# Performance work log

Measured on AMD Instinct MI355X. Metric: run time of the kernel, lower is better.

## Reference

```python
import jax, jax.numpy as jnp
import numpy as np

LN_EPS = 1e-5


def setup_inputs() -> dict:
    key = jax.random.key(0)
    k1, k2, k3, k4, k5 = jax.random.split(key, 5)
    V, D_REAL, D_HID, D_MODEL = 32000, 768, 512, 4096
    B, S = 4, 2048
    return {
        "real": jax.random.normal(k1, (V, D_REAL), dtype=jnp.float32),
        "llama_embed": jax.random.normal(k2, (V, D_MODEL), dtype=jnp.float32),
        "w1": jax.random.normal(k3, (D_HID, D_REAL), dtype=jnp.float32),  # trans_1.weight
        "w2": jax.random.normal(k4, (D_MODEL, D_HID), dtype=jnp.float32),  # trans_2.weight
        "ln_w": jnp.ones((D_HID,), dtype=jnp.float32),
        "ln_b": jnp.zeros((D_HID,), dtype=jnp.float32),
        "input_ids": jax.random.randint(k5, (B, S), 0, V, dtype=jnp.int64),
    }


def _layernorm(x, w, b):
    mu = jnp.mean(x, axis=-1, keepdims=True)
    var = jnp.mean(jnp.square(x - mu), axis=-1, keepdims=True)
    return (x - mu) * jax.lax.rsqrt(var + LN_EPS) * w + b


def reference(real, llama_embed, w1, w2, ln_w, ln_b, input_ids):
    # trans_2(ELU(LayerNorm(trans_1(real)))) over the FULL table, as in the original
    h = jnp.einsum("vd,hd->vh", real, w1)            # [V, 512]
    h = jax.nn.elu(_layernorm(h, ln_w, ln_b))        # [V, 512]
    transfered = jnp.einsum("vh,mh->vm", h, w2)      # [V, 4096]
    # gather rows per token and add frozen llama embeddings
    return transfered[input_ids] + llama_embed[input_ids]  # [B, S, 4096]
```

## Files before the change

kernel.cpp:

```cpp
#include <hip/hip_runtime.h>
#include <hip/hip_bf16.h>
#include <math.h>

#define TOKENS 8192
#define D_REAL 768
#define D_HID  512
#define D_MODEL 4096

typedef __attribute__((ext_vector_type(8))) short bf16x8;
typedef __attribute__((ext_vector_type(4))) float f32x4;

__device__ inline unsigned short f2bf(float f) {
    union { float f; unsigned u; } v; v.f = f;
    unsigned r = v.u + 0x7FFFu + ((v.u >> 16) & 1u);
    return (unsigned short)(r >> 16);
}
__device__ inline float bf2f(unsigned short h) {
    union { unsigned u; float f; } v; v.u = ((unsigned)h) << 16;
    return v.f;
}

__device__ inline void gload_lds16(const void* g, void* lds_wave_base) {
    __builtin_amdgcn_global_load_lds(
        (const __attribute__((address_space(1))) unsigned*)g,
        (__attribute__((address_space(3))) unsigned*)lds_wave_base,
        16, 0, 0);
}

__global__ __launch_bounds__(256)
void gemm1_mfma(const unsigned short* __restrict__ A,
                const unsigned short* __restrict__ B,
                unsigned short* __restrict__ C)
{
    constexpr int K = D_REAL, N = D_HID;
    __shared__ __align__(16) unsigned short As[64 * 32];
    __shared__ __align__(16) unsigned short Bs[128 * 32];

    const int tid = threadIdx.x;
    const int rowBase = blockIdx.x * 64;
    const int colBase = blockIdx.y * 128;

    const int srow = tid >> 2;
    const int scol = (tid & 3) * 8;
    const unsigned short* gA = A + (size_t)(rowBase + srow) * K + scol;
    const unsigned short* gB = B + (size_t)(colBase + srow) * K + scol;
    unsigned short* lA = As + (tid >> 6) * 512;
    unsigned short* lB = Bs + (tid >> 6) * 512;

    const int lane = tid & 63;
    const int wv   = tid >> 6;
    const int wm   = (wv >> 1) * 32;
    const int wn   = (wv & 1) * 64;
    const int frow = lane & 15;
    const int fk   = (lane >> 4) * 8;

    f32x4 acc[2][4];
    #pragma unroll
    for (int i = 0; i < 2; i++)
        #pragma unroll
        for (int j = 0; j < 4; j++) acc[i][j] = (f32x4)0.f;

    for (int k0 = 0; k0 < K; k0 += 32) {
        gload_lds16(gA,                lA);
        gload_lds16(gB,                lB);
        gload_lds16(gB + (size_t)64*K, lB + 2048);
        gA += 32; gB += 32;
        __syncthreads();

        bf16x8 af[2], bg[4];
        #pragma unroll
        for (int i = 0; i < 2; i++)
            af[i] = *reinterpret_cast<const bf16x8*>(&As[(wm + i*16 + frow) * 32 + fk]);
        #pragma unroll
        for (int j = 0; j < 4; j++)
            bg[j] = *reinterpret_cast<const bf16x8*>(&Bs[(wn + j*16 + frow) * 32 + fk]);

        #pragma unroll
        for (int i = 0; i < 2; i++)
            #pragma unroll
            for (int j = 0; j < 4; j++)
                acc[i][j] = __builtin_amdgcn_mfma_f32_16x16x32_bf16(af[i], bg[j], acc[i][j], 0, 0, 0);
        __syncthreads();
    }

    const int orow0 = wm + (lane >> 4) * 4;
    const int ocol0 = wn + frow;
    #pragma unroll
    for (int i = 0; i < 2; i++)
        #pragma unroll
        for (int r = 0; r < 4; r++) {
            unsigned short* dst = C + (size_t)(rowBase + orow0 + i*16 + r) * N + colBase + ocol0;
            #pragma unroll
            for (int j = 0; j < 4; j++)
                dst[j * 16] = f2bf(acc[i][j][r]);
        }
}

__global__ __launch_bounds__(256)
void gemm2_mfma(const unsigned short* __restrict__ A,
                const unsigned short* __restrict__ B,
                const int* __restrict__ ids,
                const float* __restrict__ embed,
                float* __restrict__ C)
{
    constexpr int K = D_HID, N = D_MODEL;
    __shared__ __align__(16) unsigned short As[128 * 32];
    __shared__ __align__(16) unsigned short Bs[128 * 32];
    __shared__ int sIds[128];

    const int f   = blockIdx.x;
    const int xcd = f & 7;
    const int idx = f >> 3;
    const int rowBase = (xcd * 8 + (idx & 7)) * 128;
    const int colBase = (idx >> 3) * 128;

    const int tid = threadIdx.x;
    if (tid < 128) sIds[tid] = ids[rowBase + tid];

    const int srow = tid >> 2;
    const int scol = (tid & 3) * 8;
    const unsigned short* gA = A + (size_t)(rowBase + srow) * K + scol;
    const unsigned short* gB = B + (size_t)(colBase + srow) * K + scol;
    unsigned short* lA = As + (tid >> 6) * 512;
    unsigned short* lB = Bs + (tid >> 6) * 512;

    const int lane = tid & 63;
    const int wv   = tid >> 6;
    const int wm   = (wv >> 1) * 64;
    const int wn   = (wv & 1) * 64;
    const int frow = lane & 15;
    const int fk   = (lane >> 4) * 8;

    f32x4 acc[4][4];
    #pragma unroll
    for (int i = 0; i < 4; i++)
        #pragma unroll
        for (int j = 0; j < 4; j++) acc[i][j] = (f32x4)0.f;

    for (int k0 = 0; k0 < K; k0 += 32) {
        gload_lds16(gA,                lA);
        gload_lds16(gA + (size_t)64*K, lA + 2048);
        gload_lds16(gB,                lB);
        gload_lds16(gB + (size_t)64*K, lB + 2048);
        gA += 32; gB += 32;
        __syncthreads();

        bf16x8 af[4], bg[4];
        #pragma unroll
        for (int i = 0; i < 4; i++)
            af[i] = *reinterpret_cast<const bf16x8*>(&As[(wm + i*16 + frow) * 32 + fk]);
        #pragma unroll
        for (int j = 0; j < 4; j++)
            bg[j] = *reinterpret_cast<const bf16x8*>(&Bs[(wn + j*16 + frow) * 32 + fk]);

        #pragma unroll
        for (int i = 0; i < 4; i++)
            #pragma unroll
            for (int j = 0; j < 4; j++)
                acc[i][j] = __builtin_amdgcn_mfma_f32_16x16x32_bf16(af[i], bg[j], acc[i][j], 0, 0, 0);
        __syncthreads();
    }

    const int orow0 = wm + (lane >> 4) * 4;
    const int ocol0 = wn + frow;
    #pragma unroll
    for (int i = 0; i < 4; i++) {
        #pragma unroll
        for (int r = 0; r < 4; r++) {
            const int lrow = orow0 + i * 16 + r;
            const size_t grow = (size_t)(rowBase + lrow);
            const float* e = embed + (size_t)sIds[lrow] * N + colBase + ocol0;
            #pragma unroll
            for (int j = 0; j < 4; j++)
                C[grow * N + colBase + ocol0 + j * 16] = acc[i][j][r] + e[j * 16];
        }
    }
}

__global__ __launch_bounds__(256)
void convert2_bf16(const float* __restrict__ s1, unsigned short* __restrict__ d1, int n1,
                   const float* __restrict__ s2, unsigned short* __restrict__ d2, int n2)
{
    int i = blockIdx.x * 256 + threadIdx.x;
    const float* src; unsigned short* dst;
    if (i < n1) { src = s1; dst = d1; }
    else {
        i -= n1;
        if (i >= n2) return;
        src = s2; dst = d2;
    }
    const float4 v = reinterpret_cast<const float4*>(src)[i];
    ushort4 o;
    o.x = f2bf(v.x); o.y = f2bf(v.y); o.z = f2bf(v.z); o.w = f2bf(v.w);
    reinterpret_cast<ushort4*>(dst)[i] = o;
}

__global__ __launch_bounds__(192)
void gather_bf16(const float* __restrict__ real, const int* __restrict__ ids,
                 unsigned short* __restrict__ Ag)
{
    const int row = blockIdx.x;
    const int t = threadIdx.x;
    const float4 v = *reinterpret_cast<const float4*>(real + (size_t)ids[row] * D_REAL + t * 4);
    ushort4 o;
    o.x = f2bf(v.x); o.y = f2bf(v.y); o.z = f2bf(v.z); o.w = f2bf(v.w);
    *reinterpret_cast<ushort4*>(Ag + (size_t)row * D_REAL + t * 4) = o;
}

__global__ __launch_bounds__(256)
void ln_elu_bf16(unsigned short* __restrict__ H,
                 const float* __restrict__ ln_w, const float* __restrict__ ln_b)
{
    const int row = blockIdx.x * 4 + (threadIdx.x >> 6);
    const int t = threadIdx.x & 63;
    unsigned short* x = H + (size_t)row * D_HID + t * 8;

    bf16x8 v = *reinterpret_cast<const bf16x8*>(x);
    float f[8], s = 0.f, ss = 0.f;
    #pragma unroll
    for (int j = 0; j < 8; j++) {
        f[j] = bf2f((unsigned short)v[j]);
        s += f[j]; ss += f[j] * f[j];
    }
    #pragma unroll
    for (int off = 32; off > 0; off >>= 1) {
        s  += __shfl_down(s, off);
        ss += __shfl_down(ss, off);
    }
    s = __shfl(s, 0); ss = __shfl(ss, 0);
    const float mu = s * (1.f / D_HID);
    const float var = ss * (1.f / D_HID) - mu * mu;
    const float rstd = rsqrtf(var + 1e-5f);

    const float4 w0 = *reinterpret_cast<const float4*>(ln_w + t * 8);
    const float4 w1 = *reinterpret_cast<const float4*>(ln_w + t * 8 + 4);
    const float4 b0 = *reinterpret_cast<const float4*>(ln_b + t * 8);
    const float4 b1 = *reinterpret_cast<const float4*>(ln_b + t * 8 + 4);
    const float wa[8] = { w0.x, w0.y, w0.z, w0.w, w1.x, w1.y, w1.z, w1.w };
    const float ba[8] = { b0.x, b0.y, b0.z, b0.w, b1.x, b1.y, b1.z, b1.w };

    bf16x8 o;
    #pragma unroll
    for (int j = 0; j < 8; j++) {
        float y = (f[j] - mu) * rstd * wa[j] + ba[j];
        y = y > 0.f ? y : expm1f(y);
        o[j] = (short)f2bf(y);
    }
    *reinterpret_cast<bf16x8*>(x) = o;
}

extern "C" void kernel_launch(void* const* d_in, const int* in_sizes, int n_in,
                              void* d_out, int out_size, void* d_ws, size_t ws_size,
                              hipStream_t stream)
{
    const float* real  = (const float*)d_in[0];
    const float* embed = (const float*)d_in[1];
    const float* w1    = (const float*)d_in[2];
    const float* w2    = (const float*)d_in[3];
    const float* ln_w  = (const float*)d_in[4];
    const float* ln_b  = (const float*)d_in[5];
    const int*   ids   = (const int*)d_in[6];
    float* out = (float*)d_out;

    unsigned short* Hb  = (unsigned short*)d_ws;
    unsigned short* w1b = Hb  + (size_t)TOKENS * D_HID;
    unsigned short* w2b = w1b + (size_t)D_HID * D_REAL;
    unsigned short* Ag  = (unsigned short*)d_out;

    const int n1 = D_HID * D_REAL / 4, n2 = D_MODEL * D_HID / 4;
    convert2_bf16<<<(n1 + n2 + 255) / 256, 256, 0, stream>>>(w1, w1b, n1, w2, w2b, n2);
    gather_bf16<<<TOKENS, 192, 0, stream>>>(real, ids, Ag);

    dim3 g1(TOKENS / 64, D_HID / 128);
    gemm1_mfma<<<g1, 256, 0, stream>>>(Ag, w1b, Hb);

    ln_elu_bf16<<<TOKENS / 4, 256, 0, stream>>>(Hb, ln_w, ln_b);

    gemm2_mfma<<<2048, 256, 0, stream>>>(Hb, w2b, ids, embed, out);
}
```

Measured before the change: 129.0 us.

## Rewrite gemm2 as 256x256 tile, double-buffered, swizzled-LDS phased MFMA pipeline

Replaces the 128x128 single-buffered gemm2 with a 512-thread kernel that computes 256x256 output tiles. K-tiles of 64 are double-buffered in LDS with an XOR swizzle, and global-to-LDS loads for the next tile are split into four phases interleaved with MFMA bursts, using manual vmcnt waits and s_setprio. The aim is to hide global load latency, cut LDS bank conflicts and raise data reuse per block. It uses 128KB of LDS per block and many accumulator registers, which limits occupancy, and with only 512 blocks the grid gives a thin tail on the GPU.

```diff
diff --git a/kernel.cpp b/kernel.cpp
--- a/kernel.cpp
+++ b/kernel.cpp
@@ -25,6 +25,12 @@
         (const __attribute__((address_space(1))) unsigned*)g,
         (__attribute__((address_space(3))) unsigned*)lds_wave_base,
         16, 0, 0);
+}
+
+__device__ inline void BAR() {
+    asm volatile("" ::: "memory");
+    __builtin_amdgcn_s_barrier();
+    asm volatile("" ::: "memory");
 }
 
 __global__ __launch_bounds__(256)
@@ -96,83 +102,130 @@
         }
 }
 
-__global__ __launch_bounds__(256)
-void gemm2_mfma(const unsigned short* __restrict__ A,
-                const unsigned short* __restrict__ B,
-                const int* __restrict__ ids,
-                const float* __restrict__ embed,
-                float* __restrict__ C)
-{
-    constexpr int K = D_HID, N = D_MODEL;
-    __shared__ __align__(16) unsigned short As[128 * 32];
-    __shared__ __align__(16) unsigned short Bs[128 * 32];
-    __shared__ int sIds[128];
+__global__ __launch_bounds__(512, 2)
+void gemm2_8phase(const unsigned short* __restrict__ A,
+                  const unsigned short* __restrict__ B,
+                  const int* __restrict__ ids,
+                  const float* __restrict__ embed,
+                  float* __restrict__ C)
+{
+    constexpr int K = D_HID, N = D_MODEL, NKT = K / 64;
+    __shared__ __align__(16) unsigned short lds[65536];
+    __shared__ int sIds[256];
+    unsigned short* Alds = lds;
+    unsigned short* Blds = lds + 32768;
 
     const int f   = blockIdx.x;
     const int xcd = f & 7;
     const int idx = f >> 3;
-    const int rowBase = (xcd * 8 + (idx & 7)) * 128;
-    const int colBase = (idx >> 3) * 128;
-
-    const int tid = threadIdx.x;
-    if (tid < 128) sIds[tid] = ids[rowBase + tid];
-
-    const int srow = tid >> 2;
-    const int scol = (tid & 3) * 8;
-    const unsigned short* gA = A + (size_t)(rowBase + srow) * K + scol;
-    const unsigned short* gB = B + (size_t)(colBase + srow) * K + scol;
-    unsigned short* lA = As + (tid >> 6) * 512;
-    unsigned short* lB = Bs + (tid >> 6) * 512;
-
+    const int rowBase = (xcd * 4 + (idx & 3)) * 256;
+    const int colBase = (idx >> 2) * 256;
+
+    const int tid  = threadIdx.x;
     const int lane = tid & 63;
     const int wv   = tid >> 6;
-    const int wm   = (wv >> 1) * 64;
-    const int wn   = (wv & 1) * 64;
+    const int wr   = wv >> 2;
+    const int wc   = wv & 3;
     const int frow = lane & 15;
-    const int fk   = (lane >> 4) * 8;
-
-    f32x4 acc[4][4];
-    #pragma unroll
-    for (int i = 0; i < 4; i++)
+    const int fq   = lane >> 4;
+
+    if (tid < 256) sIds[tid] = ids[rowBase + tid];
+
+    auto STAGE_HALF = [&](const unsigned short* Mp, unsigned short* Ml,
+                          int tileBase, int kt, int h) {
+        const int buf = kt & 1;
+        #pragma unroll
+        for (int u = 0; u < 2; ++u) {
+            const int c    = u * 512 + tid;
+            const int row  = c >> 3;
+            const int slot = (c & 7) ^ (row & 7);
+            const unsigned short* g = Mp + (size_t)(tileBase + h * 128 + row) * K
+                                         + kt * 64 + slot * 8;
+            unsigned short* l = Ml + (buf * 2 + h) * 8192 + (u * 512 + wv * 64) * 8;
+            gload_lds16(g, l);
+        }
+    };
+    auto STAGE = [&](int kt_s, int h_s) {
+        if (kt_s >= NKT) return;
+        if (h_s < 2) STAGE_HALF(A, Alds, rowBase, kt_s, h_s);
+        else         STAGE_HALF(B, Blds, colBase, kt_s, h_s - 2);
+    };
+    auto LDA = [&](int buf, int mf, int kk) -> bf16x8 {
+        const int row  = mf * 16 + frow;
+        const int slot = (kk * 4 + fq) ^ (row & 7);
+        return *reinterpret_cast<const bf16x8*>(
+            Alds + (buf * 2 + wr) * 8192 + row * 64 + slot * 8);
+    };
+    auto LDB = [&](int buf, int nf, int kk) -> bf16x8 {
+        const int rb   = wc * 64 + nf * 16 + frow;
+        const int row  = rb & 127;
+        const int slot = (kk * 4 + fq) ^ (row & 7);
+        return *reinterpret_cast<const bf16x8*>(
+            Blds + (buf * 2 + (rb >> 7)) * 8192 + row * 64 + slot * 8);
+    };
+
+    f32x4 acc[8][4];
+    #pragma unroll
+    for (int i = 0; i < 8; i++)
         #pragma unroll
         for (int j = 0; j < 4; j++) acc[i][j] = (f32x4)0.f;
 
-    for (int k0 = 0; k0 < K; k0 += 32) {
-        gload_lds16(gA,                lA);
-        gload_lds16(gA + (size_t)64*K, lA + 2048);
-        gload_lds16(gB,                lB);
-        gload_lds16(gB + (size_t)64*K, lB + 2048);
-        gA += 32; gB += 32;
-        __syncthreads();
-
-        bf16x8 af[4], bg[4];
-        #pragma unroll
-        for (int i = 0; i < 4; i++)
-            af[i] = *reinterpret_cast<const bf16x8*>(&As[(wm + i*16 + frow) * 32 + fk]);
-        #pragma unroll
-        for (int j = 0; j < 4; j++)
-            bg[j] = *reinterpret_cast<const bf16x8*>(&Bs[(wn + j*16 + frow) * 32 + fk]);
-
-        #pragma unroll
-        for (int i = 0; i < 4; i++)
-            #pragma unroll
-            for (int j = 0; j < 4; j++)
-                acc[i][j] = __builtin_amdgcn_mfma_f32_16x16x32_bf16(af[i], bg[j], acc[i][j], 0, 0, 0);
-        __syncthreads();
-    }
-
-    const int orow0 = wm + (lane >> 4) * 4;
-    const int ocol0 = wn + frow;
-    #pragma unroll
-    for (int i = 0; i < 4; i++) {
-        #pragma unroll
-        for (int r = 0; r < 4; r++) {
-            const int lrow = orow0 + i * 16 + r;
-            const size_t grow = (size_t)(rowBase + lrow);
-            const float* e = embed + (size_t)sIds[lrow] * N + colBase + ocol0;
-            #pragma unroll
-            for (int j = 0; j < 4; j++)
-                C[grow * N + colBase + ocol0 + j * 16] = acc[i][j][r] + e[j * 16];
+    STAGE(0, 0); STAGE(0, 1); STAGE(0, 2); STAGE(0, 3); STAGE(1, 0);
+    asm volatile("s_waitcnt vmcnt(2)" ::: "memory");
+    __builtin_amdgcn_s_barrier();
+    asm volatile("" ::: "memory");
+
+    #pragma unroll
+    for (int kt = 0; kt < NKT; ++kt) {
+        const int buf = kt & 1;
+        bf16x8 bg[4][2];
+        #pragma unroll
+        for (int p = 0; p < 4; ++p) {
+            bf16x8 af[2][2];
+            #pragma unroll
+            for (int i = 0; i < 2; ++i)
+                #pragma unroll
+                for (int kk = 0; kk < 2; ++kk)
+                    af[i][kk] = LDA(buf, p * 2 + i, kk);
+            if (p == 0) {
+                #pragma unroll
+                for (int nf = 0; nf < 4; ++nf)
+                    #pragma unroll
+                    for (int kk = 0; kk < 2; ++kk)
+                        bg[nf][kk] = LDB(buf, nf, kk);
+            }
+            if (p < 3) STAGE(kt + 1, p + 1);
+            BAR();
+            if (p == 3) STAGE(kt + 2, 0);
+            __builtin_amdgcn_s_setprio(1);
+            #pragma unroll
+            for (int i = 0; i < 2; ++i)
+                #pragma unroll
+                for (int nf = 0; nf < 4; ++nf)
+                    #pragma unroll
+                    for (int kk = 0; kk < 2; ++kk)
+                        acc[p*2+i][nf] = __builtin_amdgcn_mfma_f32_16x16x32_bf16(
+                            af[i][kk], bg[nf][kk], acc[p*2+i][nf], 0, 0, 0);
+            __builtin_amdgcn_s_setprio(0);
+            if (p == 3) {
+                if (kt + 2 < NKT)      asm volatile("s_waitcnt vmcnt(2)" ::: "memory");
+                else if (kt + 1 < NKT) asm volatile("s_waitcnt vmcnt(0)" ::: "memory");
+            }
+            BAR();
+        }
+    }
+
+    const int ocol0 = colBase + wc * 64 + frow;
+    #pragma unroll
+    for (int mf = 0; mf < 8; ++mf) {
+        #pragma unroll
+        for (int r = 0; r < 4; ++r) {
+            const int lrow = wr * 128 + mf * 16 + fq * 4 + r;
+            const float* e = embed + (size_t)sIds[lrow] * N + ocol0;
+            float* o = C + (size_t)(rowBase + lrow) * N + ocol0;
+            #pragma unroll
+            for (int nf = 0; nf < 4; ++nf)
+                o[nf * 16] = acc[mf][nf][r] + e[nf * 16];
         }
     }
 }
@@ -216,11 +269,11 @@
     unsigned short* x = H + (size_t)row * D_HID + t * 8;
 
     bf16x8 v = *reinterpret_cast<const bf16x8*>(x);
-    float f[8], s = 0.f, ss = 0.f;
+    float fv[8], s = 0.f, ss = 0.f;
     #pragma unroll
     for (int j = 0; j < 8; j++) {
-        f[j] = bf2f((unsigned short)v[j]);
-        s += f[j]; ss += f[j] * f[j];
+        fv[j] = bf2f((unsigned short)v[j]);
+        s += fv[j]; ss += fv[j] * fv[j];
     }
     #pragma unroll
     for (int off = 32; off > 0; off >>= 1) {
@@ -242,7 +295,7 @@
     bf16x8 o;
     #pragma unroll
     for (int j = 0; j < 8; j++) {
-        float y = (f[j] - mu) * rstd * wa[j] + ba[j];
+        float y = (fv[j] - mu) * rstd * wa[j] + ba[j];
         y = y > 0.f ? y : expm1f(y);
         o[j] = (short)f2bf(y);
     }
@@ -276,5 +329,5 @@
 
     ln_elu_bf16<<<TOKENS / 4, 256, 0, stream>>>(Hb, ln_w, ln_b);
 
-    gemm2_mfma<<<2048, 256, 0, stream>>>(Hb, w2b, ids, embed, out);
-}
+    gemm2_8phase<<<512, 512, 0, stream>>>(Hb, w2b, ids, embed, out);
+}
```

After: 124.3 us. -3.6%, faster.

## Fuse token gather into GEMM1 and enlarge GEMM2 tile to 256x128

Applied to the files above, without the earlier changes.

The separate gather/convert kernel is removed. GEMM1 now reads the fp32 rows of `real` selected by the ids directly, converts them to bf16 and stores them in LDS, which saves one launch and a full round trip of the intermediate buffer. GEMM2 moves from 128x128 to 256x128 tiles with 8x4 MFMA fragments per wave and launch_bounds(256,2), so the B tiles are reused more. The larger tile raises register pressure and halves the block count, which may hurt occupancy. The fused A load in GEMM1 goes through registers instead of async global-to-LDS, so it is no longer overlapped with the other loads.

```diff
diff --git a/kernel.cpp b/kernel.cpp
--- a/kernel.cpp
+++ b/kernel.cpp
@@ -18,6 +18,14 @@
 __device__ inline float bf2f(unsigned short h) {
     union { unsigned u; float f; } v; v.u = ((unsigned)h) << 16;
     return v.f;
+}
+__device__ inline bf16x8 cvt8(float4 a, float4 b) {
+    bf16x8 r;
+    r[0] = (short)f2bf(a.x); r[1] = (short)f2bf(a.y);
+    r[2] = (short)f2bf(a.z); r[3] = (short)f2bf(a.w);
+    r[4] = (short)f2bf(b.x); r[5] = (short)f2bf(b.y);
+    r[6] = (short)f2bf(b.z); r[7] = (short)f2bf(b.w);
+    return r;
 }
 
 __device__ inline void gload_lds16(const void* g, void* lds_wave_base) {
@@ -28,17 +36,98 @@
 }
 
 __global__ __launch_bounds__(256)
-void gemm1_mfma(const unsigned short* __restrict__ A,
+void gemm1_mfma(const float* __restrict__ real, const int* __restrict__ ids,
                 const unsigned short* __restrict__ B,
                 unsigned short* __restrict__ C)
 {
     constexpr int K = D_REAL, N = D_HID;
     __shared__ __align__(16) unsigned short As[64 * 32];
     __shared__ __align__(16) unsigned short Bs[128 * 32];
+    __shared__ int sIds[64];
 
     const int tid = threadIdx.x;
     const int rowBase = blockIdx.x * 64;
     const int colBase = blockIdx.y * 128;
+
+    if (tid < 64) sIds[tid] = ids[rowBase + tid];
+    __syncthreads();
+
+    const int srow = tid >> 2;
+    const int scol = (tid & 3) * 8;
+    const float* gA = real + (size_t)sIds[srow] * K + scol;
+    const unsigned short* gB = B + (size_t)(colBase + srow) * K + scol;
+    unsigned short* lB = Bs + (tid >> 6) * 512;
+
+    const int lane = tid & 63;
+    const int wv   = tid >> 6;
+    const int wm   = (wv >> 1) * 32;
+    const int wn   = (wv & 1) * 64;
+    const int frow = lane & 15;
+    const int fk   = (lane >> 4) * 8;
+
+    f32x4 acc[2][4];
+    #pragma unroll
+    for (int i = 0; i < 2; i++)
+        #pragma unroll
+        for (int j = 0; j < 4; j++) acc[i][j] = (f32x4)0.f;
+
+    for (int k0 = 0; k0 < K; k0 += 32) {
+        gload_lds16(gB + k0,                lB);
+        gload_lds16(gB + k0 + (size_t)64*K, lB + 2048);
+        const float4 a0 = *reinterpret_cast<const float4*>(gA + k0);
+        const float4 a1 = *reinterpret_cast<const float4*>(gA + k0 + 4);
+        *reinterpret_cast<bf16x8*>(&As[srow * 32 + scol]) = cvt8(a0, a1);
+        __syncthreads();
+
+        bf16x8 af[2], bg[4];
+        #pragma unroll
+        for (int i = 0; i < 2; i++)
+            af[i] = *reinterpret_cast<const bf16x8*>(&As[(wm + i*16 + frow) * 32 + fk]);
+        #pragma unroll
+        for (int j = 0; j < 4; j++)
+            bg[j] = *reinterpret_cast<const bf16x8*>(&Bs[(wn + j*16 + frow) * 32 + fk]);
+
+        #pragma unroll
+        for (int i = 0; i < 2; i++)
+            #pragma unroll
+            for (int j = 0; j < 4; j++)
+                acc[i][j] = __builtin_amdgcn_mfma_f32_16x16x32_bf16(af[i], bg[j], acc[i][j], 0, 0, 0);
+        __syncthreads();
+    }
+
+    const int orow0 = wm + (lane >> 4) * 4;
+    const int ocol0 = wn + frow;
+    #pragma unroll
+    for (int i = 0; i < 2; i++)
+        #pragma unroll
+        for (int r = 0; r < 4; r++) {
+            unsigned short* dst = C + (size_t)(rowBase + orow0 + i*16 + r) * N + colBase + ocol0;
+            #pragma unroll
+            for (int j = 0; j < 4; j++)
+                dst[j * 16] = f2bf(acc[i][j][r]);
+        }
+}
+
+__global__ __launch_bounds__(256, 2)
+void gemm2_mfma(const unsigned short* __restrict__ A,
+                const unsigned short* __restrict__ B,
+                const int* __restrict__ ids,
+                const float* __restrict__ embed,
+                float* __restrict__ C)
+{
+    constexpr int K = D_HID, N = D_MODEL;
+    __shared__ __align__(16) unsigned short As[256 * 32];
+    __shared__ __align__(16) unsigned short Bs[128 * 32];
+    __shared__ int sIds[256];
+
+    const int f   = blockIdx.x;
+    const int xcd = f & 7;
+    const int idx = f >> 3;
+    const int rowBase = (xcd * 4 + (idx & 3)) * 256;
+    const int colBase = (idx >> 2) * 128;
+
+    const int tid = threadIdx.x;
+    sIds[tid] = ids[rowBase + tid];
 
     const int srow = tid >> 2;
     const int scol = (tid & 3) * 8;
@@ -49,130 +138,56 @@
 
     const int lane = tid & 63;
     const int wv   = tid >> 6;
-    const int wm   = (wv >> 1) * 32;
+    const int wm   = (wv >> 1) * 128;
     const int wn   = (wv & 1) * 64;
     const int frow = lane & 15;
-    const int fk   = (lane >> 4) * 8;
-
-    f32x4 acc[2][4];
-    #pragma unroll
-    for (int i = 0; i < 2; i++)
+    const int fq   = lane >> 4;
+    const int fk   = fq * 8;
+
+    f32x4 acc[8][4];
+    #pragma unroll
+    for (int i = 0; i < 8; i++)
         #pragma unroll
         for (int j = 0; j < 4; j++) acc[i][j] = (f32x4)0.f;
 
     for (int k0 = 0; k0 < K; k0 += 32) {
-        gload_lds16(gA,                lA);
-        gload_lds16(gB,                lB);
-        gload_lds16(gB + (size_t)64*K, lB + 2048);
+        gload_lds16(gA,                 lA);
+        gload_lds16(gA + (size_t)64*K,  lA + 2048);
+        gload_lds16(gA + (size_t)128*K, lA + 4096);
+        gload_lds16(gA + (size_t)192*K, lA + 6144);
+        gload_lds16(gB,                 lB);
+        gload_lds16(gB + (size_t)64*K,  lB + 2048);
         gA += 32; gB += 32;
         __syncthreads();
 
-        bf16x8 af[2], bg[4];
-        #pragma unroll
-        for (int i = 0; i < 2; i++)
-            af[i] = *reinterpret_cast<const bf16x8*>(&As[(wm + i*16 + frow) * 32 + fk]);
-        #pragma unroll
-        for (int j = 0; j < 4; j++)
-            bg[j] = *reinterpret_cast<const bf16x8*>(&Bs[(wn + j*16 + frow) * 32 + fk]);
-
-        #pragma unroll
-        for (int i = 0; i < 2; i++)
-            #pragma unroll
-            for (int j = 0; j < 4; j++)
-                acc[i][j] = __builtin_amdgcn_mfma_f32_16x16x32_bf16(af[i], bg[j], acc[i][j], 0, 0, 0);
-        __syncthreads();
-    }
-
-    const int orow0 = wm + (lane >> 4) * 4;
-    const int ocol0 = wn + frow;
-    #pragma unroll
-    for (int i = 0; i < 2; i++)
+        bf16x8 af[8], bg[4];
+        #pragma unroll
+        for (int mf = 0; mf < 8; mf++)
+            af[mf] = *reinterpret_cast<const bf16x8*>(&As[(wm + mf*16 + frow) * 32 + fk]);
+        #pragma unroll
+        for (int nf = 0; nf < 4; nf++)
+            bg[nf] = *reinterpret_cast<const bf16x8*>(&Bs[(wn + nf*16 + frow) * 32 + fk]);
+
+        #pragma unroll
+        for (int mf = 0; mf < 8; mf++)
+            #pragma unroll
+            for (int nf = 0; nf < 4; nf++)
+                acc[mf][nf] = __builtin_amdgcn_mfma_f32_16x16x32_bf16(
+                    af[mf], bg[nf], acc[mf][nf], 0, 0, 0);
+        __syncthreads();
+    }
+
+    const int ocol0 = colBase + wn + frow;
+    #pragma unroll
+    for (int mf = 0; mf < 8; mf++) {
         #pragma unroll
         for (int r = 0; r < 4; r++) {
-            unsigned short* dst = C + (size_t)(rowBase + orow0 + i*16 + r) * N + colBase + ocol0;
-            #pragma unroll
-            for (int j = 0; j < 4; j++)
-                dst[j * 16] = f2bf(acc[i][j][r]);
-        }
-}
-
-__global__ __launch_bounds__(256)
-void gemm2_mfma(const unsigned short* __restrict__ A,
-                const unsigned short* __restrict__ B,
-                const int* __restrict__ ids,
-                const float* __restrict__ embed,
-                float* __restrict__ C)
-{
-    constexpr int K = D_HID, N = D_MODEL;
-    __shared__ __align__(16) unsigned short As[128 * 32];
-    __shared__ __align__(16) unsigned short Bs[128 * 32];
-    __shared__ int sIds[128];
-
-    const int f   = blockIdx.x;
-    const int xcd = f & 7;
-    const int idx = f >> 3;
-    const int rowBase = (xcd * 8 + (idx & 7)) * 128;
-    const int colBase = (idx >> 3) * 128;
-
-    const int tid = threadIdx.x;
-    if (tid < 128) sIds[tid] = ids[rowBase + tid];
-
-    const int srow = tid >> 2;
-    const int scol = (tid & 3) * 8;
-    const unsigned short* gA = A + (size_t)(rowBase + srow) * K + scol;
-    const unsigned short* gB = B + (size_t)(colBase + srow) * K + scol;
-    unsigned short* lA = As + (tid >> 6) * 512;
-    unsigned short* lB = Bs + (tid >> 6) * 512;
-
-    const int lane = tid & 63;
-    const int wv   = tid >> 6;
-    const int wm   = (wv >> 1) * 64;
-    const int wn   = (wv & 1) * 64;
-    const int frow = lane & 15;
-    const int fk   = (lane >> 4) * 8;
-
-    f32x4 acc[4][4];
-    #pragma unroll
-    for (int i = 0; i < 4; i++)
-        #pragma unroll
-        for (int j = 0; j < 4; j++) acc[i][j] = (f32x4)0.f;
-
-    for (int k0 = 0; k0 < K; k0 += 32) {
-        gload_lds16(gA,                lA);
-        gload_lds16(gA + (size_t)64*K, lA + 2048);
-        gload_lds16(gB,                lB);
-        gload_lds16(gB + (size_t)64*K, lB + 2048);
-        gA += 32; gB += 32;
-        __syncthreads();
-
-        bf16x8 af[4], bg[4];
-        #pragma unroll
-        for (int i = 0; i < 4; i++)
-            af[i] = *reinterpret_cast<const bf16x8*>(&As[(wm + i*16 + frow) * 32 + fk]);
-        #pragma unroll
-        for (int j = 0; j < 4; j++)
-            bg[j] = *reinterpret_cast<const bf16x8*>(&Bs[(wn + j*16 + frow) * 32 + fk]);
-
-        #pragma unroll
-        for (int i = 0; i < 4; i++)
-            #pragma unroll
-            for (int j = 0; j < 4; j++)
-                acc[i][j] = __builtin_amdgcn_mfma_f32_16x16x32_bf16(af[i], bg[j], acc[i][j], 0, 0, 0);
-        __syncthreads();
-    }
-
-    const int orow0 = wm + (lane >> 4) * 4;
-    const int ocol0 = wn + frow;
-    #pragma unroll
-    for (int i = 0; i < 4; i++) {
-        #pragma unroll
-        for (int r = 0; r < 4; r++) {
-            const int lrow = orow0 + i * 16 + r;
-            const size_t grow = (size_t)(rowBase + lrow);
-            const float* e = embed + (size_t)sIds[lrow] * N + colBase + ocol0;
-            #pragma unroll
-            for (int j = 0; j < 4; j++)
-                C[grow * N + colBase + ocol0 + j * 16] = acc[i][j][r] + e[j * 16];
+            const int lrow = wm + mf * 16 + fq * 4 + r;
+            const float* e = embed + (size_t)sIds[lrow] * N + ocol0;
+            float* o = C + (size_t)(rowBase + lrow) * N + ocol0;
+            #pragma unroll
+            for (int nf = 0; nf < 4; nf++)
+                o[nf * 16] = acc[mf][nf][r] + e[nf * 16];
         }
     }
 }
@@ -195,18 +210,6 @@
     reinterpret_cast<ushort4*>(dst)[i] = o;
 }
 
-__global__ __launch_bounds__(192)
-void gather_bf16(const float* __restrict__ real, const int* __restrict__ ids,
-                 unsigned short* __restrict__ Ag)
-{
-    const int row = blockIdx.x;
-    const int t = threadIdx.x;
-    const float4 v = *reinterpret_cast<const float4*>(real + (size_t)ids[row] * D_REAL + t * 4);
-    ushort4 o;
-    o.x = f2bf(v.x); o.y = f2bf(v.y); o.z = f2bf(v.z); o.w = f2bf(v.w);
-    *reinterpret_cast<ushort4*>(Ag + (size_t)row * D_REAL + t * 4) = o;
-}
-
 __global__ __launch_bounds__(256)
 void ln_elu_bf16(unsigned short* __restrict__ H,
                  const float* __restrict__ ln_w, const float* __restrict__ ln_b)
@@ -216,11 +219,11 @@
     unsigned short* x = H + (size_t)row * D_HID + t * 8;
 
     bf16x8 v = *reinterpret_cast<const bf16x8*>(x);
-    float f[8], s = 0.f, ss = 0.f;
+    float fv[8], s = 0.f, ss = 0.f;
     #pragma unroll
     for (int j = 0; j < 8; j++) {
-        f[j] = bf2f((unsigned short)v[j]);
-        s += f[j]; ss += f[j] * f[j];
+        fv[j] = bf2f((unsigned short)v[j]);
+        s += fv[j]; ss += fv[j] * fv[j];
     }
     #pragma unroll
     for (int off = 32; off > 0; off >>= 1) {
@@ -242,7 +245,7 @@
     bf16x8 o;
     #pragma unroll
     for (int j = 0; j < 8; j++) {
-        float y = (f[j] - mu) * rstd * wa[j] + ba[j];
+        float y = (fv[j] - mu) * rstd * wa[j] + ba[j];
         y = y > 0.f ? y : expm1f(y);
         o[j] = (short)f2bf(y);
     }
@@ -265,16 +268,14 @@
     unsigned short* Hb  = (unsigned short*)d_ws;
     unsigned short* w1b = Hb  + (size_t)TOKENS * D_HID;
     unsigned short* w2b = w1b + (size_t)D_HID * D_REAL;
-    unsigned short* Ag  = (unsigned short*)d_out;
 
     const int n1 = D_HID * D_REAL / 4, n2 = D_MODEL * D_HID / 4;
     convert2_bf16<<<(n1 + n2 + 255) / 256, 256, 0, stream>>>(w1, w1b, n1, w2, w2b, n2);
-    gather_bf16<<<TOKENS, 192, 0, stream>>>(real, ids, Ag);
 
     dim3 g1(TOKENS / 64, D_HID / 128);
-    gemm1_mfma<<<g1, 256, 0, stream>>>(Ag, w1b, Hb);
+    gemm1_mfma<<<g1, 256, 0, stream>>>(real, ids, w1b, Hb);
 
     ln_elu_bf16<<<TOKENS / 4, 256, 0, stream>>>(Hb, ln_w, ln_b);
 
-    gemm2_mfma<<<2048, 256, 0, stream>>>(Hb, w2b, ids, embed, out);
-}
+    gemm2_mfma<<<1024, 256, 0, stream>>>(Hb, w2b, ids, embed, out);
+}
```

Result: slower. 134.1 us (+3.9%).

## Fuse row gather and bf16 cast into GEMM1, prefetch embeddings in GEMM2 loop

Applied to the files above, without the earlier changes.

Removes the separate gather kernel: GEMM1 now reads the fp32 rows of `real` through token ids, converts them to bf16 in registers and writes them to LDS. GEMM2 loads the llama embedding values for its epilogue inside the k-loop, so those latencies overlap with MFMA work instead of stalling the store phase, and it declares a launch bound of 2 blocks. The cost is extra registers for the prefetched embeddings and synchronous A loads in GEMM1 in place of async global-to-LDS loads. GEMM1 now also reads the `real` row 4 times, once per column block, instead of once.

```diff
diff --git a/kernel.cpp b/kernel.cpp
--- a/kernel.cpp
+++ b/kernel.cpp
@@ -18,6 +18,14 @@
 __device__ inline float bf2f(unsigned short h) {
     union { unsigned u; float f; } v; v.u = ((unsigned)h) << 16;
     return v.f;
+}
+__device__ inline bf16x8 cvt8(float4 a, float4 b) {
+    bf16x8 r;
+    r[0] = (short)f2bf(a.x); r[1] = (short)f2bf(a.y);
+    r[2] = (short)f2bf(a.z); r[3] = (short)f2bf(a.w);
+    r[4] = (short)f2bf(b.x); r[5] = (short)f2bf(b.y);
+    r[6] = (short)f2bf(b.z); r[7] = (short)f2bf(b.w);
+    return r;
 }
 
 __device__ inline void gload_lds16(const void* g, void* lds_wave_base) {
@@ -28,17 +36,99 @@
 }
 
 __global__ __launch_bounds__(256)
-void gemm1_mfma(const unsigned short* __restrict__ A,
+void gemm1_mfma(const float* __restrict__ real, const int* __restrict__ ids,
                 const unsigned short* __restrict__ B,
                 unsigned short* __restrict__ C)
 {
     constexpr int K = D_REAL, N = D_HID;
     __shared__ __align__(16) unsigned short As[64 * 32];
     __shared__ __align__(16) unsigned short Bs[128 * 32];
+    __shared__ int sIds[64];
 
     const int tid = threadIdx.x;
     const int rowBase = blockIdx.x * 64;
     const int colBase = blockIdx.y * 128;
+
+    if (tid < 64) sIds[tid] = ids[rowBase + tid];
+    __syncthreads();
+
+    const int srow = tid >> 2;
+    const int scol = (tid & 3) * 8;
+    const float* gA = real + (size_t)sIds[srow] * K + scol;
+    const unsigned short* gB = B + (size_t)(colBase + srow) * K + scol;
+    unsigned short* lB = Bs + (tid >> 6) * 512;
+
+    const int lane = tid & 63;
+    const int wv   = tid >> 6;
+    const int wm   = (wv >> 1) * 32;
+    const int wn   = (wv & 1) * 64;
+    const int frow = lane & 15;
+    const int fk   = (lane >> 4) * 8;
+
+    f32x4 acc[2][4];
+    #pragma unroll
+    for (int i = 0; i < 2; i++)
+        #pragma unroll
+        for (int j = 0; j < 4; j++) acc[i][j] = (f32x4)0.f;
+
+    for (int k0 = 0; k0 < K; k0 += 32) {
+        gload_lds16(gB + k0,                lB);
+        gload_lds16(gB + k0 + (size_t)64*K, lB + 2048);
+        const float4 a0 = *reinterpret_cast<const float4*>(gA + k0);
+        const float4 a1 = *reinterpret_cast<const float4*>(gA + k0 + 4);
+        *reinterpret_cast<bf16x8*>(&As[srow * 32 + scol]) = cvt8(a0, a1);
+        __syncthreads();
+
+        bf16x8 af[2], bg[4];
+        #pragma unroll
+        for (int i = 0; i < 2; i++)
+            af[i] = *reinterpret_cast<const bf16x8*>(&As[(wm + i*16 + frow) * 32 + fk]);
+        #pragma unroll
+        for (int j = 0; j < 4; j++)
+            bg[j] = *reinterpret_cast<const bf16x8*>(&Bs[(wn + j*16 + frow) * 32 + fk]);
+
+        #pragma unroll
+        for (int i = 0; i < 2; i++)
+            #pragma unroll
+            for (int j = 0; j < 4; j++)
+                acc[i][j] = __builtin_amdgcn_mfma_f32_16x16x32_bf16(af[i], bg[j], acc[i][j], 0, 0, 0);
+        __syncthreads();
+    }
+
+    const int orow0 = wm + (lane >> 4) * 4;
+    const int ocol0 = wn + frow;
+    #pragma unroll
+    for (int i = 0; i < 2; i++)
+        #pragma unroll
+        for (int r = 0; r < 4; r++) {
+            unsigned short* dst = C + (size_t)(rowBase + orow0 + i*16 + r) * N + colBase + ocol0;
+            #pragma unroll
+            for (int j = 0; j < 4; j++)
+                dst[j * 16] = f2bf(acc[i][j][r]);
+        }
+}
+
+__global__ __launch_bounds__(256, 2)
+void gemm2_mfma(const unsigned short* __restrict__ A,
+                const unsigned short* __restrict__ B,
+                const int* __restrict__ ids,
+                const float* __restrict__ embed,
+                float* __restrict__ C)
+{
+    constexpr int K = D_HID, N = D_MODEL;
+    __shared__ __align__(16) unsigned short As[128 * 32];
+    __shared__ __align__(16) unsigned short Bs[128 * 32];
+    __shared__ int sIds[128];
+
+    const int f   = blockIdx.x;
+    const int xcd = f & 7;
+    const int idx = f >> 3;
+    const int rowBase = (xcd * 8 + (idx & 7)) * 128;
+    const int colBase = (idx >> 3) * 128;
+
+    const int tid = threadIdx.x;
+    if (tid < 128) sIds[tid] = ids[rowBase + tid];
+    __syncthreads();
 
     const int srow = tid >> 2;
     const int scol = (tid & 3) * 8;
@@ -49,100 +139,38 @@
 
     const int lane = tid & 63;
     const int wv   = tid >> 6;
-    const int wm   = (wv >> 1) * 32;
-    const int wn   = (wv & 1) * 64;
-    const int frow = lane & 15;
-    const int fk   = (lane >> 4) * 8;
-
-    f32x4 acc[2][4];
-    #pragma unroll
-    for (int i = 0; i < 2; i++)
-        #pragma unroll
-        for (int j = 0; j < 4; j++) acc[i][j] = (f32x4)0.f;
-
-    for (int k0 = 0; k0 < K; k0 += 32) {
-        gload_lds16(gA,                lA);
-        gload_lds16(gB,                lB);
-        gload_lds16(gB + (size_t)64*K, lB + 2048);
-        gA += 32; gB += 32;
-        __syncthreads();
-
-        bf16x8 af[2], bg[4];
-        #pragma unroll
-        for (int i = 0; i < 2; i++)
-            af[i] = *reinterpret_cast<const bf16x8*>(&As[(wm + i*16 + frow) * 32 + fk]);
-        #pragma unroll
-        for (int j = 0; j < 4; j++)
-            bg[j] = *reinterpret_cast<const bf16x8*>(&Bs[(wn + j*16 + frow) * 32 + fk]);
-
-        #pragma unroll
-        for (int i = 0; i < 2; i++)
-            #pragma unroll
-            for (int j = 0; j < 4; j++)
-                acc[i][j] = __builtin_amdgcn_mfma_f32_16x16x32_bf16(af[i], bg[j], acc[i][j], 0, 0, 0);
-        __syncthreads();
-    }
-
-    const int orow0 = wm + (lane >> 4) * 4;
-    const int ocol0 = wn + frow;
-    #pragma unroll
-    for (int i = 0; i < 2; i++)
-        #pragma unroll
-        for (int r = 0; r < 4; r++) {
-            unsigned short* dst = C + (size_t)(rowBase + orow0 + i*16 + r) * N + colBase + ocol0;
-            #pragma unroll
-            for (int j = 0; j < 4; j++)
-                dst[j * 16] = f2bf(acc[i][j][r]);
-        }
-}
-
-__global__ __launch_bounds__(256)
-void gemm2_mfma(const unsigned short* __restrict__ A,
-                const unsigned short* __restrict__ B,
-                const int* __restrict__ ids,
-                const float* __restrict__ embed,
-                float* __restrict__ C)
-{
-    constexpr int K = D_HID, N = D_MODEL;
-    __shared__ __align__(16) unsigned short As[128 * 32];
-    __shared__ __align__(16) unsigned short Bs[128 * 32];
-    __shared__ int sIds[128];
-
-    const int f   = blockIdx.x;
-    const int xcd = f & 7;
-    const int idx = f >> 3;
-    const int rowBase = (xcd * 8 + (idx & 7)) * 128;
-    const int colBase = (idx >> 3) * 128;
-
-    const int tid = threadIdx.x;
-    if (tid < 128) sIds[tid] = ids[rowBase + tid];
-
-    const int srow = tid >> 2;
-    const int scol = (tid & 3) * 8;
-    const unsigned short* gA = A + (size_t)(rowBase + srow) * K + scol;
-    const unsigned short* gB = B + (size_t)(colBase + srow) * K + scol;
-    unsigned short* lA = As + (tid >> 6) * 512;
-    unsigned short* lB = Bs + (tid >> 6) * 512;
-
-    const int lane = tid & 63;
-    const int wv   = tid >> 6;
     const int wm   = (wv >> 1) * 64;
     const int wn   = (wv & 1) * 64;
     const int frow = lane & 15;
     const int fk   = (lane >> 4) * 8;
 
+    const int orow0 = wm + (lane >> 4) * 4;
+    const int ocol0 = wn + frow;
+
     f32x4 acc[4][4];
     #pragma unroll
     for (int i = 0; i < 4; i++)
         #pragma unroll
         for (int j = 0; j < 4; j++) acc[i][j] = (f32x4)0.f;
 
-    for (int k0 = 0; k0 < K; k0 += 32) {
+    float epre[4][4][4];
+
+    #pragma unroll
+    for (int s = 0; s < 16; ++s) {
         gload_lds16(gA,                lA);
         gload_lds16(gA + (size_t)64*K, lA + 2048);
         gload_lds16(gB,                lB);
         gload_lds16(gB + (size_t)64*K, lB + 2048);
         gA += 32; gB += 32;
+
+        {
+            const int pi = s >> 2, pr = s & 3;
+            const int lrow = orow0 + pi * 16 + pr;
+            const float* e = embed + (size_t)sIds[lrow] * N + colBase + ocol0;
+            #pragma unroll
+            for (int j = 0; j < 4; ++j)
+                epre[pi][pr][j] = e[j * 16];
+        }
         __syncthreads();
 
         bf16x8 af[4], bg[4];
@@ -161,18 +189,15 @@
         __syncthreads();
     }
 
-    const int orow0 = wm + (lane >> 4) * 4;
-    const int ocol0 = wn + frow;
     #pragma unroll
     for (int i = 0; i < 4; i++) {
         #pragma unroll
         for (int r = 0; r < 4; r++) {
             const int lrow = orow0 + i * 16 + r;
-            const size_t grow = (size_t)(rowBase + lrow);
-            const float* e = embed + (size_t)sIds[lrow] * N + colBase + ocol0;
-            #pragma unroll
-            for (int j = 0; j < 4; j++)
-                C[grow * N + colBase + ocol0 + j * 16] = acc[i][j][r] + e[j * 16];
+            float* o = C + (size_t)(rowBase + lrow) * N + colBase + ocol0;
+            #pragma unroll
+            for (int j = 0; j < 4; j++)
+                o[j * 16] = acc[i][j][r] + epre[i][r][j];
         }
     }
 }
@@ -195,18 +220,6 @@
     reinterpret_cast<ushort4*>(dst)[i] = o;
 }
 
-__global__ __launch_bounds__(192)
-void gather_bf16(const float* __restrict__ real, const int* __restrict__ ids,
-                 unsigned short* __restrict__ Ag)
-{
-    const int row = blockIdx.x;
-    const int t = threadIdx.x;
-    const float4 v = *reinterpret_cast<const float4*>(real + (size_t)ids[row] * D_REAL + t * 4);
-    ushort4 o;
-    o.x = f2bf(v.x); o.y = f2bf(v.y); o.z = f2bf(v.z); o.w = f2bf(v.w);
-    *reinterpret_cast<ushort4*>(Ag + (size_t)row * D_REAL + t * 4) = o;
-}
-
 __global__ __launch_bounds__(256)
 void ln_elu_bf16(unsigned short* __restrict__ H,
                  const float* __restrict__ ln_w, const float* __restrict__ ln_b)
@@ -216,11 +229,11 @@
     unsigned short* x = H + (size_t)row * D_HID + t * 8;
 
     bf16x8 v = *reinterpret_cast<const bf16x8*>(x);
-    float f[8], s = 0.f, ss = 0.f;
+    float fv[8], s = 0.f, ss = 0.f;
     #pragma unroll
     for (int j = 0; j < 8; j++) {
-        f[j] = bf2f((unsigned short)v[j]);
-        s += f[j]; ss += f[j] * f[j];
+        fv[j] = bf2f((unsigned short)v[j]);
+        s += fv[j]; ss += fv[j] * fv[j];
     }
     #pragma unroll
     for (int off = 32; off > 0; off >>= 1) {
@@ -242,7 +255,7 @@
     bf16x8 o;
     #pragma unroll
     for (int j = 0; j < 8; j++) {
-        float y = (f[j] - mu) * rstd * wa[j] + ba[j];
+        float y = (fv[j] - mu) * rstd * wa[j] + ba[j];
         y = y > 0.f ? y : expm1f(y);
         o[j] = (short)f2bf(y);
     }
@@ -265,14 +278,12 @@
     unsigned short* Hb  = (unsigned short*)d_ws;
     unsigned short* w1b = Hb  + (size_t)TOKENS * D_HID;
     unsigned short* w2b = w1b + (size_t)D_HID * D_REAL;
-    unsigned short* Ag  = (unsigned short*)d_out;
 
     const int n1 = D_HID * D_REAL / 4, n2 = D_MODEL * D_HID / 4;
     convert2_bf16<<<(n1 + n2 + 255) / 256, 256, 0, stream>>>(w1, w1b, n1, w2, w2b, n2);
-    gather_bf16<<<TOKENS, 192, 0, stream>>>(real, ids, Ag);
 
     dim3 g1(TOKENS / 64, D_HID / 128);
-    gemm1_mfma<<<g1, 256, 0, stream>>>(Ag, w1b, Hb);
+    gemm1_mfma<<<g1, 256, 0, stream>>>(real, ids, w1b, Hb);
 
     ln_elu_bf16<<<TOKENS / 4, 256, 0, stream>>>(Hb, ln_w, ln_b);
 
```

Measured after the change: 143.4 us. 11.1% more time.
